# Optimization experiments

Hardware: AMD Instinct MI355X
Metric: run time of the kernel (lower is better)

The kernel has to match this reference:

```python
import jax, jax.numpy as jnp
import numpy as np

N_QUBITS = 5
N_LAYERS = 3
DIM = 2 ** N_QUBITS  # 32


def _apply_ry(state, theta, w):
    # state: [B, 32] complex64; theta: scalar or [B] float32
    half = theta * 0.5
    c = jnp.cos(half)
    s = jnp.sin(half)
    if c.ndim:  # per-sample angles
        c = c[:, None, None]
        s = s[:, None, None]
    pre, post = 2 ** w, 2 ** (N_QUBITS - 1 - w)
    st = state.reshape(-1, pre, 2, post)
    s0, s1 = st[:, :, 0, :], st[:, :, 1, :]
    out = jnp.stack([c * s0 - s * s1, s * s0 + c * s1], axis=2)
    return out.reshape(-1, DIM)


def _apply_rz(state, theta, w):
    half = theta * 0.5
    e0 = jnp.exp(-1j * half)
    e1 = jnp.exp(1j * half)
    pre, post = 2 ** w, 2 ** (N_QUBITS - 1 - w)
    st = state.reshape(-1, pre, 2, post)
    out = jnp.stack([e0 * st[:, :, 0, :], e1 * st[:, :, 1, :]], axis=2)
    return out.reshape(-1, DIM)


def _apply_cnot(state, c):
    # control wire c, target wire c+1 (adjacent, as in the CNOT chain)
    pre, post = 2 ** c, 2 ** (N_QUBITS - 2 - c)
    st = state.reshape(-1, pre, 2, 2, post)
    out = jnp.stack([st[:, :, 0], st[:, :, 1, ::-1, :]], axis=2)
    return out.reshape(-1, DIM)


def _expval_z(state, w):
    pre, post = 2 ** w, 2 ** (N_QUBITS - 1 - w)
    p = jnp.abs(state.reshape(-1, pre, 2, post)) ** 2
    return (p[:, :, 0, :] - p[:, :, 1, :]).sum(axis=(1, 2))


def _circuit(enc, qp):
    # enc: [B, 5] in [-1,1]; qp: [30]
    B = enc.shape[0]
    state = jnp.zeros((B, DIM), jnp.complex64).at[:, 0].set(1.0)
    pi = jnp.float32(np.pi)
    for i in range(N_QUBITS):
        state = _apply_ry(state, enc[:, i] * pi, i)
    idx = 0
    for _ in range(N_LAYERS):
        for i in range(N_QUBITS):
            state = _apply_ry(state, qp[idx], i); idx += 1
            state = _apply_rz(state, qp[idx], i); idx += 1
        for i in range(N_QUBITS - 1):
            state = _apply_cnot(state, i)
    return jnp.stack([_expval_z(state, i) for i in range(N_QUBITS)], axis=1)


def setup_inputs() -> dict:
    key = jax.random.key(0)
    ks = jax.random.split(key, 14)
    B, S, A = 131072, 252, 4
    def lin(k, fin, fout):
        return jax.random.normal(k, (fin, fout), jnp.float32) / jnp.sqrt(jnp.float32(fin))
    return {
        'state': jax.random.normal(ks[0], (B, S), jnp.float32),
        'W1': lin(ks[1], S, 128), 'b1': jnp.zeros((128,), jnp.float32),
        'W2': lin(ks[2], 128, 64), 'b2': jnp.zeros((64,), jnp.float32),
        'W3': lin(ks[3], 64, N_QUBITS), 'b3': jnp.zeros((N_QUBITS,), jnp.float32),
        'qp': jax.random.normal(ks[4], (N_LAYERS * N_QUBITS * 2,), jnp.float32) * 0.1,
        'D1': lin(ks[5], N_QUBITS, 32), 'd1': jnp.zeros((32,), jnp.float32),
        'D2': lin(ks[6], 32, 16), 'd2': jnp.zeros((16,), jnp.float32),
        'D3': lin(ks[7], 16, A), 'd3': jnp.zeros((A,), jnp.float32),
    }


def reference(state, W1, b1, W2, b2, W3, b3, qp, D1, d1, D2, d2, D3, d3):
    h = jax.nn.relu(state @ W1 + b1)
    h = jax.nn.relu(h @ W2 + b2)
    enc = jnp.tanh(h @ W3 + b3)          # [B, 5]
    q = _circuit(enc, qp)                # [B, 5] PauliZ expectations
    h = jax.nn.relu(q @ D1 + d1)
    h = jax.nn.relu(h @ D2 + d2)
    return h @ D3 + d3                   # [B, action_dim]
```

## Files before the change

kernel.cpp:

```cpp
#include <hip/hip_runtime.h>
#include <hip/hip_bf16.h>
#include <math.h>

typedef _Float16 half8_t __attribute__((ext_vector_type(8)));
typedef _Float16 half4_t __attribute__((ext_vector_type(4)));
typedef float floatx4 __attribute__((ext_vector_type(4)));

#define TPT 8

__device__ __forceinline__ void lds_barrier() {
    asm volatile("s_waitcnt lgkmcnt(0)" ::: "memory");
    __builtin_amdgcn_s_barrier();
    asm volatile("" ::: "memory");
}

__device__ __forceinline__ float fast_tanh(float x) {
    float e = __expf(2.f * x);
    return 1.f - 2.f / (e + 1.f);
}

__device__ __forceinline__ void prep_body(const float* __restrict__ W,
                                          _Float16* __restrict__ dst,
                                          int K, int N, int KS, int b) {
    int ks   = b % KS;
    int nt   = b / KS;
    int lane = threadIdx.x;
    int col  = nt * 16 + (lane & 15);
    int kbase = ks * 32 + ((lane >> 4) << 3);
    half8_t v;
#pragma unroll
    for (int j = 0; j < 8; ++j) {
        int k = kbase + j;
        float x = (k < K && col < N) ? W[(size_t)k * N + col] : 0.f;
        v[j] = (_Float16)x;
    }
    *(half8_t*)(dst + (size_t)(b * 64 + lane) * 8) = v;
}

__global__ void prep_all(const float* __restrict__ W1, const float* __restrict__ W2,
                         const float* __restrict__ W3,
                         _Float16* __restrict__ w1f, _Float16* __restrict__ w2f,
                         _Float16* __restrict__ w3f) {
    int b = blockIdx.x;
    if (b < 64)      prep_body(W1, w1f, 252, 128, 8, b);
    else if (b < 80) prep_body(W2, w2f, 128, 64, 4, b - 64);
    else             prep_body(W3, w3f, 64, 5, 2, b - 80);
}

__global__ __launch_bounds__(256, 2) void front_kernel(
    const float* __restrict__ state,
    const _Float16* __restrict__ w1f, const float* __restrict__ b1,
    const _Float16* __restrict__ w2f, const float* __restrict__ b2,
    const _Float16* __restrict__ w3f, const float* __restrict__ b3,
    float* __restrict__ enc, int Btot) {
    __shared__ char lds[28672];
    const int tid = threadIdx.x;
    const int w   = tid >> 6;
    const int l   = tid & 63;
    const int l15 = l & 15;
    const int lhi = l >> 4;
    const int row0 = blockIdx.x * (32 * TPT);

    const int srow = tid >> 3;
    const int sc0  = tid & 7;
    const int sswz = (srow & 7) << 4;

    floatx4 pf[8];

#define ISSUE_A(T)                                                          \
    {                                                                       \
        const float* Ar = state + (size_t)(row0 + (T) * 32 + srow) * 252;   \
        _Pragma("unroll")                                                   \
        for (int jj = 0; jj < 8; ++jj) {                                    \
            int c = sc0 + jj * 8;                                           \
            if (c < 63) pf[jj] = *(const floatx4*)(Ar + c * 4);             \
        }                                                                   \
    }

    ISSUE_A(0)

    half8_t bw1[2][8], bw2[4], bw3[2];
#pragma unroll
    for (int ntl = 0; ntl < 2; ++ntl)
#pragma unroll
        for (int ks = 0; ks < 8; ++ks)
            bw1[ntl][ks] = *(const half8_t*)(w1f + (size_t)(((w * 2 + ntl) * 8 + ks) * 64 + l) * 8);
#pragma unroll
    for (int ks = 0; ks < 4; ++ks)
        bw2[ks] = *(const half8_t*)(w2f + (size_t)((w * 4 + ks) * 64 + l) * 8);
#pragma unroll
    for (int ks = 0; ks < 2; ++ks)
        bw3[ks] = *(const half8_t*)(w3f + (size_t)(ks * 64 + l) * 8);

#pragma unroll 1
    for (int t = 0; t < TPT; ++t) {
#pragma unroll
        for (int jj = 0; jj < 8; ++jj) {
            int c = sc0 + jj * 8;
            half4_t h;
            if (c == 63) {
                h = half4_t{0, 0, 0, 0};
            } else {
                floatx4 f = pf[jj];
                h = half4_t{ (_Float16)f[0], (_Float16)f[1], (_Float16)f[2], (_Float16)f[3] };
            }
            *(half4_t*)(lds + (srow << 9) + ((c * 8) ^ sswz)) = h;
        }
        if (t + 1 < TPT) ISSUE_A(t + 1)
        lds_barrier();

        floatx4 acc1[2][2];
#pragma unroll
        for (int mi = 0; mi < 2; ++mi)
#pragma unroll
            for (int ntl = 0; ntl < 2; ++ntl) acc1[mi][ntl] = floatx4{0, 0, 0, 0};
#pragma unroll
        for (int ks = 0; ks < 8; ++ks) {
            half8_t a[2];
#pragma unroll
            for (int mi = 0; mi < 2; ++mi) {
                int r = mi * 16 + l15;
                int cb = ks * 64 + lhi * 16;
                a[mi] = *(const half8_t*)(lds + (r << 9) + (cb ^ ((r & 7) << 4)));
            }
#pragma unroll
            for (int mi = 0; mi < 2; ++mi)
#pragma unroll
                for (int ntl = 0; ntl < 2; ++ntl)
                    acc1[mi][ntl] = __builtin_amdgcn_mfma_f32_16x16x32_f16(a[mi], bw1[ntl][ks], acc1[mi][ntl], 0, 0, 0);
        }

#pragma unroll
        for (int ntl = 0; ntl < 2; ++ntl) {
            int col = (w * 2 + ntl) * 16 + l15;
            float bb = b1[col];
#pragma unroll
            for (int mi = 0; mi < 2; ++mi)
#pragma unroll
                for (int ri = 0; ri < 4; ++ri) {
                    int row = mi * 16 + lhi * 4 + ri;
                    float v = acc1[mi][ntl][ri] + bb;
                    v = v > 0.f ? v : 0.f;
                    *(_Float16*)(lds + 16384 + (row << 8) + ((col * 2) ^ ((row & 7) << 4))) = (_Float16)v;
                }
        }
        lds_barrier();

        floatx4 acc2[2];
#pragma unroll
        for (int mi = 0; mi < 2; ++mi) acc2[mi] = floatx4{0, 0, 0, 0};
#pragma unroll
        for (int ks = 0; ks < 4; ++ks)
#pragma unroll
            for (int mi = 0; mi < 2; ++mi) {
                int r = mi * 16 + l15;
                int cb = ks * 64 + lhi * 16;
                half8_t a = *(const half8_t*)(lds + 16384 + (r << 8) + (cb ^ ((r & 7) << 4)));
                acc2[mi] = __builtin_amdgcn_mfma_f32_16x16x32_f16(a, bw2[ks], acc2[mi], 0, 0, 0);
            }

        {
            int col = w * 16 + l15;
            float bb = b2[col];
#pragma unroll
            for (int mi = 0; mi < 2; ++mi)
#pragma unroll
                for (int ri = 0; ri < 4; ++ri) {
                    int row = mi * 16 + lhi * 4 + ri;
                    float v = acc2[mi][ri] + bb;
                    v = v > 0.f ? v : 0.f;
                    *(_Float16*)(lds + 24576 + (row << 7) + ((col * 2) ^ ((row & 7) << 4))) = (_Float16)v;
                }
        }
        lds_barrier();

        if (w < 2) {
            floatx4 acc3 = floatx4{0, 0, 0, 0};
#pragma unroll
            for (int ks = 0; ks < 2; ++ks) {
                int r = w * 16 + l15;
                int cb = ks * 64 + lhi * 16;
                half8_t a = *(const half8_t*)(lds + 24576 + (r << 7) + (cb ^ ((r & 7) << 4)));
                acc3 = __builtin_amdgcn_mfma_f32_16x16x32_f16(a, bw3[ks], acc3, 0, 0, 0);
            }
            if (l15 < 5) {
                float bb = b3[l15];
#pragma unroll
                for (int ri = 0; ri < 4; ++ri) {
                    int grow = row0 + t * 32 + w * 16 + lhi * 4 + ri;
                    enc[(size_t)l15 * Btot + grow] = fast_tanh(acc3[ri] + bb);
                }
            }
        }
    }
#undef ISSUE_A
}

template<int P>
__device__ __forceinline__ void ry_g(float* re, float* im, float c, float s) {
    constexpr int STR = 1 << P;
#pragma unroll
    for (int base = 0; base < 32; base += 2 * STR)
#pragma unroll
        for (int d = 0; d < STR; ++d) {
            int i0 = base + d, i1 = i0 + STR;
            float r0 = re[i0], r1 = re[i1], m0 = im[i0], m1 = im[i1];
            re[i0] = c * r0 - s * r1;  re[i1] = s * r0 + c * r1;
            im[i0] = c * m0 - s * m1;  im[i1] = s * m0 + c * m1;
        }
}

template<int P>
__device__ __forceinline__ void rz_g(float* re, float* im, float c, float s) {
#pragma unroll
    for (int i = 0; i < 32; ++i) {
        float t = ((i >> P) & 1) ? s : -s;
        float r = re[i], m = im[i];
        re[i] = c * r - t * m;
        im[i] = c * m + t * r;
    }
}

template<int PC, int PT>
__device__ __forceinline__ void cnot_g(float* re, float* im) {
#pragma unroll
    for (int i = 0; i < 32; ++i) {
        if (((i >> PC) & 1) && !((i >> PT) & 1)) {
            int j = i | (1 << PT);
            float t;
            t = re[i]; re[i] = re[j]; re[j] = t;
            t = im[i]; im[i] = im[j]; im[j] = t;
        }
    }
}

__global__ __launch_bounds__(256) void back_kernel(
    const float* __restrict__ enc, const float* __restrict__ qp,
    const float* __restrict__ D1, const float* __restrict__ d1,
    const float* __restrict__ D2, const float* __restrict__ d2,
    const float* __restrict__ D3, const float* __restrict__ d3,
    float* __restrict__ out, int Btot) {
    __shared__ float sD1[160], sd1[32], sD2[512], sd2[16], sD3[64], sd3[4];
    __shared__ float sQc[30], sQs[30];
    const int tid = threadIdx.x;
    for (int i = tid; i < 512; i += 256) sD2[i] = D2[i];
    if (tid < 160) sD1[tid] = D1[tid];
    if (tid < 32)  sd1[tid] = d1[tid];
    if (tid < 64)  sD3[tid] = D3[tid];
    if (tid < 16)  sd2[tid] = d2[tid];
    if (tid < 4)   sd3[tid] = d3[tid];
    if (tid < 30) { float h = 0.5f * qp[tid]; sQc[tid] = cosf(h); sQs[tid] = sinf(h); }
    __syncthreads();

    const size_t r = (size_t)blockIdx.x * 256 + tid;

    float cq[5], sq[5];
    const float HPI = 1.57079632679489662f;
#pragma unroll
    for (int i = 0; i < 5; ++i) {
        float a = enc[(size_t)i * Btot + r] * HPI;
        cq[i] = __cosf(a);
        sq[i] = __sinf(a);
    }
    float re[32], im[32];
#pragma unroll
    for (int i = 0; i < 32; ++i) {
        float v = ((i >> 4) & 1) ? sq[0] : cq[0];
        v *= ((i >> 3) & 1) ? sq[1] : cq[1];
        v *= ((i >> 2) & 1) ? sq[2] : cq[2];
        v *= ((i >> 1) & 1) ? sq[3] : cq[3];
        v *= ( i       & 1) ? sq[4] : cq[4];
        re[i] = v;
        im[i] = 0.f;
    }

#pragma unroll
    for (int lay = 0; lay < 3; ++lay) {
        const float* c = sQc + lay * 10;
        const float* s = sQs + lay * 10;
        ry_g<4>(re, im, c[0], s[0]);  rz_g<4>(re, im, c[1], s[1]);
        ry_g<3>(re, im, c[2], s[2]);  rz_g<3>(re, im, c[3], s[3]);
        ry_g<2>(re, im, c[4], s[4]);  rz_g<2>(re, im, c[5], s[5]);
        ry_g<1>(re, im, c[6], s[6]);  rz_g<1>(re, im, c[7], s[7]);
        ry_g<0>(re, im, c[8], s[8]);  rz_g<0>(re, im, c[9], s[9]);
        cnot_g<4, 3>(re, im);
        cnot_g<3, 2>(re, im);
        cnot_g<2, 1>(re, im);
        cnot_g<1, 0>(re, im);
    }

    float q[5] = {0, 0, 0, 0, 0};
#pragma unroll
    for (int i = 0; i < 32; ++i) {
        float p = re[i] * re[i] + im[i] * im[i];
        q[0] += ((i >> 4) & 1) ? -p : p;
        q[1] += ((i >> 3) & 1) ? -p : p;
        q[2] += ((i >> 2) & 1) ? -p : p;
        q[3] += ((i >> 1) & 1) ? -p : p;
        q[4] += ( i       & 1) ? -p : p;
    }

    float h1[32];
#pragma unroll
    for (int j = 0; j < 32; ++j) {
        float a = sd1[j];
#pragma unroll
        for (int k = 0; k < 5; ++k) a += q[k] * sD1[k * 32 + j];
        h1[j] = a > 0.f ? a : 0.f;
    }
    float h2[16];
#pragma unroll
    for (int j = 0; j < 16; ++j) {
        float a = sd2[j];
#pragma unroll
        for (int k = 0; k < 32; ++k) a += h1[k] * sD2[k * 16 + j];
        h2[j] = a > 0.f ? a : 0.f;
    }
    floatx4 o;
#pragma unroll
    for (int j = 0; j < 4; ++j) {
        float a = sd3[j];
#pragma unroll
        for (int k = 0; k < 16; ++k) a += h2[k] * sD3[k * 4 + j];
        o[j] = a;
    }
    *(floatx4*)(out + r * 4) = o;
}

extern "C" void kernel_launch(void* const* d_in, const int* in_sizes, int n_in,
                              void* d_out, int out_size, void* d_ws, size_t ws_size,
                              hipStream_t stream) {
    const float* state = (const float*)d_in[0];
    const float* W1 = (const float*)d_in[1];
    const float* b1 = (const float*)d_in[2];
    const float* W2 = (const float*)d_in[3];
    const float* b2 = (const float*)d_in[4];
    const float* W3 = (const float*)d_in[5];
    const float* b3 = (const float*)d_in[6];
    const float* qp = (const float*)d_in[7];
    const float* D1 = (const float*)d_in[8];
    const float* d1 = (const float*)d_in[9];
    const float* D2 = (const float*)d_in[10];
    const float* d2 = (const float*)d_in[11];
    const float* D3 = (const float*)d_in[12];
    const float* d3 = (const float*)d_in[13];
    float* out = (float*)d_out;

    const int B = in_sizes[0] / 252;

    char* ws = (char*)d_ws;
    _Float16* w1f = (_Float16*)ws;
    _Float16* w2f = (_Float16*)(ws + 65536);
    _Float16* w3f = (_Float16*)(ws + 65536 + 16384);
    float*    enc = (float*)(ws + 65536 + 16384 + 2048);

    prep_all<<<82, 64, 0, stream>>>(W1, W2, W3, w1f, w2f, w3f);
    front_kernel<<<B / (32 * TPT), 256, 0, stream>>>(state, w1f, b1, w2f, b2, w3f, b3, enc, B);
    back_kernel<<<B / 256, 256, 0, stream>>>(enc, qp, D1, d1, D2, d2, D3, d3, out, B);
}
```

Baseline: 56.46 us.

## Split front MLP across 8 waves and stage W2/W3 fragments in LDS

The front kernel goes from 256 to 512 threads per block. Each wave now owns one 16-column tile of layer 1, so it holds 8 W1 fragments instead of 16 in registers. W2 and W3 weight fragments move from registers into LDS, and layer-2 work is split across 8 waves by row and column tile. The goal is fewer VGPRs per thread and higher occupancy (launch bounds 512,4) to hide the latency of streaming the input. The cost is larger LDS use per block and extra LDS reads for B fragments in layers 2 and 3.

```diff
diff --git a/kernel.cpp b/kernel.cpp
--- a/kernel.cpp
+++ b/kernel.cpp
@@ -47,13 +47,13 @@
     else             prep_body(W3, w3f, 64, 5, 2, b - 80);
 }
 
-__global__ __launch_bounds__(256, 2) void front_kernel(
+__global__ __launch_bounds__(512, 4) void front_kernel(
     const float* __restrict__ state,
     const _Float16* __restrict__ w1f, const float* __restrict__ b1,
     const _Float16* __restrict__ w2f, const float* __restrict__ b2,
     const _Float16* __restrict__ w3f, const float* __restrict__ b3,
     float* __restrict__ enc, int Btot) {
-    __shared__ char lds[28672];
+    __shared__ char lds[47104];
     const int tid = threadIdx.x;
     const int w   = tid >> 6;
     const int l   = tid & 63;
@@ -61,42 +61,51 @@
     const int lhi = l >> 4;
     const int row0 = blockIdx.x * (32 * TPT);
 
-    const int srow = tid >> 3;
-    const int sc0  = tid & 7;
+    const int srow = tid >> 4;
+    const int sc0  = tid & 15;
     const int sswz = (srow & 7) << 4;
 
-    floatx4 pf[8];
+    floatx4 pf[4];
 
 #define ISSUE_A(T)                                                          \
     {                                                                       \
         const float* Ar = state + (size_t)(row0 + (T) * 32 + srow) * 252;   \
         _Pragma("unroll")                                                   \
-        for (int jj = 0; jj < 8; ++jj) {                                    \
-            int c = sc0 + jj * 8;                                           \
+        for (int jj = 0; jj < 4; ++jj) {                                    \
+            int c = sc0 + jj * 16;                                          \
             if (c < 63) pf[jj] = *(const floatx4*)(Ar + c * 4);             \
         }                                                                   \
     }
 
     ISSUE_A(0)
 
-    half8_t bw1[2][8], bw2[4], bw3[2];
-#pragma unroll
-    for (int ntl = 0; ntl < 2; ++ntl)
-#pragma unroll
-        for (int ks = 0; ks < 8; ++ks)
-            bw1[ntl][ks] = *(const half8_t*)(w1f + (size_t)(((w * 2 + ntl) * 8 + ks) * 64 + l) * 8);
-#pragma unroll
-    for (int ks = 0; ks < 4; ++ks)
-        bw2[ks] = *(const half8_t*)(w2f + (size_t)((w * 4 + ks) * 64 + l) * 8);
-#pragma unroll
-    for (int ks = 0; ks < 2; ++ks)
-        bw3[ks] = *(const half8_t*)(w3f + (size_t)(ks * 64 + l) * 8);
+    half8_t bw1[8];
+#pragma unroll
+    for (int ks = 0; ks < 8; ++ks)
+        bw1[ks] = *(const half8_t*)(w1f + (size_t)((w * 8 + ks) * 64 + l) * 8);
+
+    {
+        const floatx4* s2 = (const floatx4*)w2f;
+        *(floatx4*)(lds + 28672 + tid * 16)        = s2[tid];
+        *(floatx4*)(lds + 28672 + 8192 + tid * 16) = s2[512 + tid];
+        if (tid < 128) {
+            const floatx4* s3 = (const floatx4*)w3f;
+            *(floatx4*)(lds + 45056 + tid * 16) = s3[tid];
+        }
+    }
+
+    const float bb1 = b1[w * 16 + l15];
+    const float bb2 = b2[(w & 3) * 16 + l15];
+    const float bb3 = b3[l15 < 5 ? l15 : 4];
+
+    const int mi2 = w >> 2;
+    const int nt2 = w & 3;
 
 #pragma unroll 1
     for (int t = 0; t < TPT; ++t) {
 #pragma unroll
-        for (int jj = 0; jj < 8; ++jj) {
-            int c = sc0 + jj * 8;
+        for (int jj = 0; jj < 4; ++jj) {
+            int c = sc0 + jj * 16;
             half4_t h;
             if (c == 63) {
                 h = half4_t{0, 0, 0, 0};
@@ -109,68 +118,51 @@
         if (t + 1 < TPT) ISSUE_A(t + 1)
         lds_barrier();
 
-        floatx4 acc1[2][2];
-#pragma unroll
-        for (int mi = 0; mi < 2; ++mi)
-#pragma unroll
-            for (int ntl = 0; ntl < 2; ++ntl) acc1[mi][ntl] = floatx4{0, 0, 0, 0};
+        floatx4 acc1[2] = { floatx4{0, 0, 0, 0}, floatx4{0, 0, 0, 0} };
 #pragma unroll
         for (int ks = 0; ks < 8; ++ks) {
-            half8_t a[2];
+            int cb = ks * 64 + lhi * 16;
 #pragma unroll
             for (int mi = 0; mi < 2; ++mi) {
                 int r = mi * 16 + l15;
-                int cb = ks * 64 + lhi * 16;
-                a[mi] = *(const half8_t*)(lds + (r << 9) + (cb ^ ((r & 7) << 4)));
-            }
-#pragma unroll
-            for (int mi = 0; mi < 2; ++mi)
-#pragma unroll
-                for (int ntl = 0; ntl < 2; ++ntl)
-                    acc1[mi][ntl] = __builtin_amdgcn_mfma_f32_16x16x32_f16(a[mi], bw1[ntl][ks], acc1[mi][ntl], 0, 0, 0);
-        }
-
-#pragma unroll
-        for (int ntl = 0; ntl < 2; ++ntl) {
-            int col = (w * 2 + ntl) * 16 + l15;
-            float bb = b1[col];
+                half8_t a = *(const half8_t*)(lds + (r << 9) + (cb ^ ((r & 7) << 4)));
+                acc1[mi] = __builtin_amdgcn_mfma_f32_16x16x32_f16(a, bw1[ks], acc1[mi], 0, 0, 0);
+            }
+        }
+
+        {
+            int col2 = (w * 16 + l15) * 2;
 #pragma unroll
             for (int mi = 0; mi < 2; ++mi)
 #pragma unroll
                 for (int ri = 0; ri < 4; ++ri) {
                     int row = mi * 16 + lhi * 4 + ri;
-                    float v = acc1[mi][ntl][ri] + bb;
+                    float v = acc1[mi][ri] + bb1;
                     v = v > 0.f ? v : 0.f;
-                    *(_Float16*)(lds + 16384 + (row << 8) + ((col * 2) ^ ((row & 7) << 4))) = (_Float16)v;
+                    *(_Float16*)(lds + 16384 + (row << 8) + (col2 ^ ((row & 7) << 4))) = (_Float16)v;
                 }
         }
         lds_barrier();
 
-        floatx4 acc2[2];
-#pragma unroll
-        for (int mi = 0; mi < 2; ++mi) acc2[mi] = floatx4{0, 0, 0, 0};
-#pragma unroll
-        for (int ks = 0; ks < 4; ++ks)
-#pragma unroll
-            for (int mi = 0; mi < 2; ++mi) {
-                int r = mi * 16 + l15;
-                int cb = ks * 64 + lhi * 16;
-                half8_t a = *(const half8_t*)(lds + 16384 + (r << 8) + (cb ^ ((r & 7) << 4)));
-                acc2[mi] = __builtin_amdgcn_mfma_f32_16x16x32_f16(a, bw2[ks], acc2[mi], 0, 0, 0);
-            }
+        floatx4 acc2 = floatx4{0, 0, 0, 0};
+#pragma unroll
+        for (int ks = 0; ks < 4; ++ks) {
+            int r = mi2 * 16 + l15;
+            int cb = ks * 64 + lhi * 16;
+            half8_t a  = *(const half8_t*)(lds + 16384 + (r << 8) + (cb ^ ((r & 7) << 4)));
+            half8_t bf = *(const half8_t*)(lds + 28672 + ((nt2 * 4 + ks) * 64 + l) * 16);
+            acc2 = __builtin_amdgcn_mfma_f32_16x16x32_f16(a, bf, acc2, 0, 0, 0);
+        }
 
         {
-            int col = w * 16 + l15;
-            float bb = b2[col];
-#pragma unroll
-            for (int mi = 0; mi < 2; ++mi)
-#pragma unroll
-                for (int ri = 0; ri < 4; ++ri) {
-                    int row = mi * 16 + lhi * 4 + ri;
-                    float v = acc2[mi][ri] + bb;
-                    v = v > 0.f ? v : 0.f;
-                    *(_Float16*)(lds + 24576 + (row << 7) + ((col * 2) ^ ((row & 7) << 4))) = (_Float16)v;
-                }
+            int col2 = (nt2 * 16 + l15) * 2;
+#pragma unroll
+            for (int ri = 0; ri < 4; ++ri) {
+                int row = mi2 * 16 + lhi * 4 + ri;
+                float v = acc2[ri] + bb2;
+                v = v > 0.f ? v : 0.f;
+                *(_Float16*)(lds + 24576 + (row << 7) + (col2 ^ ((row & 7) << 4))) = (_Float16)v;
+            }
         }
         lds_barrier();
 
@@ -180,15 +172,15 @@
             for (int ks = 0; ks < 2; ++ks) {
                 int r = w * 16 + l15;
                 int cb = ks * 64 + lhi * 16;
-                half8_t a = *(const half8_t*)(lds + 24576 + (r << 7) + (cb ^ ((r & 7) << 4)));
-                acc3 = __builtin_amdgcn_mfma_f32_16x16x32_f16(a, bw3[ks], acc3, 0, 0, 0);
+                half8_t a  = *(const half8_t*)(lds + 24576 + (r << 7) + (cb ^ ((r & 7) << 4)));
+                half8_t bf = *(const half8_t*)(lds + 45056 + (ks * 64 + l) * 16);
+                acc3 = __builtin_amdgcn_mfma_f32_16x16x32_f16(a, bf, acc3, 0, 0, 0);
             }
             if (l15 < 5) {
-                float bb = b3[l15];
 #pragma unroll
                 for (int ri = 0; ri < 4; ++ri) {
                     int grow = row0 + t * 32 + w * 16 + lhi * 4 + ri;
-                    enc[(size_t)l15 * Btot + grow] = fast_tanh(acc3[ri] + bb);
+                    enc[(size_t)l15 * Btot + grow] = fast_tanh(acc3[ri] + bb3);
                 }
             }
         }
@@ -355,6 +347,6 @@
     float*    enc = (float*)(ws + 65536 + 16384 + 2048);
 
     prep_all<<<82, 64, 0, stream>>>(W1, W2, W3, w1f, w2f, w3f);
-    front_kernel<<<B / (32 * TPT), 256, 0, stream>>>(state, w1f, b1, w2f, b2, w3f, b3, enc, B);
+    front_kernel<<<B / (32 * TPT), 512, 0, stream>>>(state, w1f, b1, w2f, b2, w3f, b3, enc, B);
     back_kernel<<<B / 256, 256, 0, stream>>>(enc, qp, D1, d1, D2, d2, D3, d3, out, B);
 }
```

After: 55.78 us. No clear change (-1.2%).

## Widen front MLP block to 512 threads with 2D warp tiling over 64 rows

Applied to the files above, without the earlier changes.

The front kernel now uses 8 waves per block handling 64 rows per tile. Waves are split into a 4x2 grid over rows and output columns, so each A fragment read from LDS feeds four MFMAs instead of two. Layer biases are hoisted out of the loop, and the W3 fragments are staged in LDS rather than held in registers. This cuts LDS reads and the per-wave weight register footprint relative to work done, but raises LDS use to about 58KB per block and 512 threads per block, which may limit occupancy.

```diff
diff --git a/kernel.cpp b/kernel.cpp
--- a/kernel.cpp
+++ b/kernel.cpp
@@ -47,19 +47,21 @@
     else             prep_body(W3, w3f, 64, 5, 2, b - 80);
 }
 
-__global__ __launch_bounds__(256, 2) void front_kernel(
+__global__ __launch_bounds__(512, 2) void front_kernel(
     const float* __restrict__ state,
     const _Float16* __restrict__ w1f, const float* __restrict__ b1,
     const _Float16* __restrict__ w2f, const float* __restrict__ b2,
     const _Float16* __restrict__ w3f, const float* __restrict__ b3,
     float* __restrict__ enc, int Btot) {
-    __shared__ char lds[28672];
+    __shared__ char lds[59392];
     const int tid = threadIdx.x;
     const int w   = tid >> 6;
     const int l   = tid & 63;
     const int l15 = l & 15;
     const int lhi = l >> 4;
-    const int row0 = blockIdx.x * (32 * TPT);
+    const int mw  = w >> 1;
+    const int nw  = w & 1;
+    const int row0 = blockIdx.x * (64 * TPT);
 
     const int srow = tid >> 3;
     const int sc0  = tid & 7;
@@ -69,7 +71,7 @@
 
 #define ISSUE_A(T)                                                          \
     {                                                                       \
-        const float* Ar = state + (size_t)(row0 + (T) * 32 + srow) * 252;   \
+        const float* Ar = state + (size_t)(row0 + (T) * 64 + srow) * 252;   \
         _Pragma("unroll")                                                   \
         for (int jj = 0; jj < 8; ++jj) {                                    \
             int c = sc0 + jj * 8;                                           \
@@ -79,18 +81,31 @@
 
     ISSUE_A(0)
 
-    half8_t bw1[2][8], bw2[4], bw3[2];
+    half8_t bw1[4][8];
+#pragma unroll
+    for (int ntl = 0; ntl < 4; ++ntl)
+#pragma unroll
+        for (int ks = 0; ks < 8; ++ks)
+            bw1[ntl][ks] = *(const half8_t*)(w1f + (size_t)(((nw * 4 + ntl) * 8 + ks) * 64 + l) * 8);
+
+    half8_t bw2[2][4];
 #pragma unroll
     for (int ntl = 0; ntl < 2; ++ntl)
 #pragma unroll
-        for (int ks = 0; ks < 8; ++ks)
-            bw1[ntl][ks] = *(const half8_t*)(w1f + (size_t)(((w * 2 + ntl) * 8 + ks) * 64 + l) * 8);
-#pragma unroll
-    for (int ks = 0; ks < 4; ++ks)
-        bw2[ks] = *(const half8_t*)(w2f + (size_t)((w * 4 + ks) * 64 + l) * 8);
-#pragma unroll
-    for (int ks = 0; ks < 2; ++ks)
-        bw3[ks] = *(const half8_t*)(w3f + (size_t)(ks * 64 + l) * 8);
+        for (int ks = 0; ks < 4; ++ks)
+            bw2[ntl][ks] = *(const half8_t*)(w2f + (size_t)(((nw * 2 + ntl) * 4 + ks) * 64 + l) * 8);
+
+    if (tid < 128) {
+        const floatx4* s3 = (const floatx4*)w3f;
+        *(floatx4*)(lds + 57344 + tid * 16) = s3[tid];
+    }
+
+    float bb1[4], bb2[2];
+#pragma unroll
+    for (int ntl = 0; ntl < 4; ++ntl) bb1[ntl] = b1[(nw * 4 + ntl) * 16 + l15];
+#pragma unroll
+    for (int ntl = 0; ntl < 2; ++ntl) bb2[ntl] = b2[(nw * 2 + ntl) * 16 + l15];
+    const float bb3 = b3[l15 < 5 ? l15 : 4];
 
 #pragma unroll 1
     for (int t = 0; t < TPT; ++t) {
@@ -109,86 +124,71 @@
         if (t + 1 < TPT) ISSUE_A(t + 1)
         lds_barrier();
 
-        floatx4 acc1[2][2];
-#pragma unroll
-        for (int mi = 0; mi < 2; ++mi)
-#pragma unroll
-            for (int ntl = 0; ntl < 2; ++ntl) acc1[mi][ntl] = floatx4{0, 0, 0, 0};
+        floatx4 acc1[4];
+#pragma unroll
+        for (int ntl = 0; ntl < 4; ++ntl) acc1[ntl] = floatx4{0, 0, 0, 0};
 #pragma unroll
         for (int ks = 0; ks < 8; ++ks) {
-            half8_t a[2];
-#pragma unroll
-            for (int mi = 0; mi < 2; ++mi) {
-                int r = mi * 16 + l15;
-                int cb = ks * 64 + lhi * 16;
-                a[mi] = *(const half8_t*)(lds + (r << 9) + (cb ^ ((r & 7) << 4)));
-            }
-#pragma unroll
-            for (int mi = 0; mi < 2; ++mi)
-#pragma unroll
-                for (int ntl = 0; ntl < 2; ++ntl)
-                    acc1[mi][ntl] = __builtin_amdgcn_mfma_f32_16x16x32_f16(a[mi], bw1[ntl][ks], acc1[mi][ntl], 0, 0, 0);
+            int r = mw * 16 + l15;
+            int cb = ks * 64 + lhi * 16;
+            half8_t a = *(const half8_t*)(lds + (r << 9) + (cb ^ ((r & 7) << 4)));
+#pragma unroll
+            for (int ntl = 0; ntl < 4; ++ntl)
+                acc1[ntl] = __builtin_amdgcn_mfma_f32_16x16x32_f16(a, bw1[ntl][ks], acc1[ntl], 0, 0, 0);
+        }
+
+#pragma unroll
+        for (int ntl = 0; ntl < 4; ++ntl) {
+            int col2 = ((nw * 4 + ntl) * 16 + l15) * 2;
+#pragma unroll
+            for (int ri = 0; ri < 4; ++ri) {
+                int row = mw * 16 + lhi * 4 + ri;
+                float v = acc1[ntl][ri] + bb1[ntl];
+                v = v > 0.f ? v : 0.f;
+                *(_Float16*)(lds + 32768 + (row << 8) + (col2 ^ ((row & 7) << 4))) = (_Float16)v;
+            }
+        }
+        lds_barrier();
+
+        floatx4 acc2[2] = { floatx4{0, 0, 0, 0}, floatx4{0, 0, 0, 0} };
+#pragma unroll
+        for (int ks = 0; ks < 4; ++ks) {
+            int r = mw * 16 + l15;
+            int cb = ks * 64 + lhi * 16;
+            half8_t a = *(const half8_t*)(lds + 32768 + (r << 8) + (cb ^ ((r & 7) << 4)));
+#pragma unroll
+            for (int ntl = 0; ntl < 2; ++ntl)
+                acc2[ntl] = __builtin_amdgcn_mfma_f32_16x16x32_f16(a, bw2[ntl][ks], acc2[ntl], 0, 0, 0);
         }
 
 #pragma unroll
         for (int ntl = 0; ntl < 2; ++ntl) {
-            int col = (w * 2 + ntl) * 16 + l15;
-            float bb = b1[col];
-#pragma unroll
-            for (int mi = 0; mi < 2; ++mi)
-#pragma unroll
-                for (int ri = 0; ri < 4; ++ri) {
-                    int row = mi * 16 + lhi * 4 + ri;
-                    float v = acc1[mi][ntl][ri] + bb;
-                    v = v > 0.f ? v : 0.f;
-                    *(_Float16*)(lds + 16384 + (row << 8) + ((col * 2) ^ ((row & 7) << 4))) = (_Float16)v;
-                }
+            int col2 = ((nw * 2 + ntl) * 16 + l15) * 2;
+#pragma unroll
+            for (int ri = 0; ri < 4; ++ri) {
+                int row = mw * 16 + lhi * 4 + ri;
+                float v = acc2[ntl][ri] + bb2[ntl];
+                v = v > 0.f ? v : 0.f;
+                *(_Float16*)(lds + 49152 + (row << 7) + (col2 ^ ((row & 7) << 4))) = (_Float16)v;
+            }
         }
         lds_barrier();
 
-        floatx4 acc2[2];
-#pragma unroll
-        for (int mi = 0; mi < 2; ++mi) acc2[mi] = floatx4{0, 0, 0, 0};
-#pragma unroll
-        for (int ks = 0; ks < 4; ++ks)
-#pragma unroll
-            for (int mi = 0; mi < 2; ++mi) {
-                int r = mi * 16 + l15;
-                int cb = ks * 64 + lhi * 16;
-                half8_t a = *(const half8_t*)(lds + 16384 + (r << 8) + (cb ^ ((r & 7) << 4)));
-                acc2[mi] = __builtin_amdgcn_mfma_f32_16x16x32_f16(a, bw2[ks], acc2[mi], 0, 0, 0);
-            }
-
-        {
-            int col = w * 16 + l15;
-            float bb = b2[col];
-#pragma unroll
-            for (int mi = 0; mi < 2; ++mi)
-#pragma unroll
-                for (int ri = 0; ri < 4; ++ri) {
-                    int row = mi * 16 + lhi * 4 + ri;
-                    float v = acc2[mi][ri] + bb;
-                    v = v > 0.f ? v : 0.f;
-                    *(_Float16*)(lds + 24576 + (row << 7) + ((col * 2) ^ ((row & 7) << 4))) = (_Float16)v;
-                }
-        }
-        lds_barrier();
-
-        if (w < 2) {
+        if (w < 4) {
             floatx4 acc3 = floatx4{0, 0, 0, 0};
 #pragma unroll
             for (int ks = 0; ks < 2; ++ks) {
                 int r = w * 16 + l15;
                 int cb = ks * 64 + lhi * 16;
-                half8_t a = *(const half8_t*)(lds + 24576 + (r << 7) + (cb ^ ((r & 7) << 4)));
-                acc3 = __builtin_amdgcn_mfma_f32_16x16x32_f16(a, bw3[ks], acc3, 0, 0, 0);
+                half8_t a  = *(const half8_t*)(lds + 49152 + (r << 7) + (cb ^ ((r & 7) << 4)));
+                half8_t bf = *(const half8_t*)(lds + 57344 + (ks * 64 + l) * 16);
+                acc3 = __builtin_amdgcn_mfma_f32_16x16x32_f16(a, bf, acc3, 0, 0, 0);
             }
             if (l15 < 5) {
-                float bb = b3[l15];
 #pragma unroll
                 for (int ri = 0; ri < 4; ++ri) {
-                    int grow = row0 + t * 32 + w * 16 + lhi * 4 + ri;
-                    enc[(size_t)l15 * Btot + grow] = fast_tanh(acc3[ri] + bb);
+                    int grow = row0 + t * 64 + w * 16 + lhi * 4 + ri;
+                    enc[(size_t)l15 * Btot + grow] = fast_tanh(acc3[ri] + bb3);
                 }
             }
         }
@@ -355,6 +355,6 @@
     float*    enc = (float*)(ws + 65536 + 16384 + 2048);
 
     prep_all<<<82, 64, 0, stream>>>(W1, W2, W3, w1f, w2f, w3f);
-    front_kernel<<<B / (32 * TPT), 256, 0, stream>>>(state, w1f, b1, w2f, b2, w3f, b3, enc, B);
+    front_kernel<<<B / (64 * TPT), 512, 0, stream>>>(state, w1f, b1, w2f, b2, w3f, b3, enc, B);
     back_kernel<<<B / 256, 256, 0, stream>>>(enc, qp, D1, d1, D2, d2, D3, d3, out, B);
 }
```

Measured after the change: 76.01 us. 34.6% more time.
